# Kernel tuning notes

Hardware: AMD Instinct MI355X
Metric: run time of the kernel (lower is better)

## Reference

```python
import jax, jax.numpy as jnp
import numpy as np

N = 10000      # nodes
E = 320000     # edges (avg degree 32)
C = 256        # feature dim (input_dim == output_dim)
L = 3          # num_layers
D = 20         # KAF dictionary size
BOUNDARY = 4.0 # KAF dictionary boundary


def setup_inputs() -> dict:
    key = jax.random.key(0)
    ks = jax.random.split(key, 7)
    x = jax.random.normal(ks[0], (N, C), jnp.float32)
    edge_index = jax.random.randint(ks[1], (2, E), 0, N, jnp.int32)
    edge_attr = jax.random.normal(ks[2], (E, 2), jnp.float32)
    # per-layer stacked parameters (all layers have identical shapes)
    node_w = jax.random.normal(ks[3], (L, C, C), jnp.float32) / jnp.sqrt(jnp.float32(C))
    edge_w = jax.random.normal(ks[4], (L, 2, C), jnp.float32) / jnp.sqrt(jnp.float32(2))
    neigh_w = jax.random.normal(ks[5], (L, C, C), jnp.float32) / jnp.sqrt(jnp.float32(C))
    bias = jnp.zeros((L, C), jnp.float32)
    alpha = jax.random.normal(ks[6], (L, C, D), jnp.float32) * 0.3
    return dict(x=x, edge_index=edge_index, edge_attr=edge_attr,
                node_w=node_w, edge_w=edge_w, neigh_w=neigh_w, bias=bias, alpha=alpha)


def _kaf(s, alpha_l):
    # Kernel Activation Function (Scardapane et al.): per-channel Gaussian mixture
    dict_pts = jnp.linspace(-BOUNDARY, BOUNDARY, D, dtype=s.dtype)  # [D]
    interval = 2.0 * BOUNDARY / (D - 1)
    gamma = 0.5 / (2.0 * interval) ** 2
    K = jnp.exp(-gamma * jnp.square(s[..., None] - dict_pts))  # [N, C, D]
    return jnp.einsum('ncd,cd->nc', K, alpha_l)


def reference(x, edge_index, edge_attr, node_w, edge_w, neigh_w, bias, alpha):
    src, dst = edge_index[0], edge_index[1]
    # mean-aggregation normalizer (computed once; graph is fixed across layers)
    cnt = jax.ops.segment_sum(jnp.ones((E,), x.dtype), dst, num_segments=N)
    inv_cnt = jnp.where(cnt > 0, 1.0 / jnp.maximum(cnt, 1.0), 0.0)  # [N]
    h = x
    for l in range(L):
        # message: edge_attr @ W_e + x_j @ W_n  -> [E, C]
        msg = edge_attr @ edge_w[l] + h[src] @ neigh_w[l]
        # mean aggregate to destination nodes
        aggr = jax.ops.segment_sum(msg, dst, num_segments=N) * inv_cnt[:, None]
        # update: KAF(aggr + x @ W + b)
        h = _kaf(aggr + h @ node_w[l] + bias[l], alpha[l])
    return h
```

## Files before the change

### kernel.cpp

```cpp
#include <hip/hip_runtime.h>
#include <hip/hip_bf16.h>

#define N_NODES 10000
#define N_EDGES 320000
#define CDIM    256
#define B_PRE   80
#define EPB     (N_EDGES / B_PRE)
#define SLK     130
#define SA      84

typedef __attribute__((ext_vector_type(8))) _Float16 half8;
typedef __attribute__((ext_vector_type(4))) _Float16 half4;
typedef __attribute__((ext_vector_type(4))) float floatx4;

#define OFF_RS    0
#define OFF_INVC  40960
#define OFF_S2    81920
#define OFF_COLV  163840
#define OFF_WCAT  806912
#define OFF_HN    1593344
#define OFF_HX    6713344
#define OFF_PERC  OFF_HN
#define OFF_BASE  (OFF_HN + 1600000)
#define OFF_EA2   OFF_HX
#define OFF_CTOT  (OFF_HX + 2560000)

__global__ __launch_bounds__(256) void k_prep(const float4* __restrict__ x, half4* __restrict__ hB,
                                              const float* __restrict__ neigh_w, const float* __restrict__ node_w,
                                              _Float16* __restrict__ wcatT) {
  __shared__ float t[32][33];
  const int b = blockIdx.x;
  if (b < 2500) {
    int i = b * 256 + threadIdx.x;
    float4 v = x[i];
    half4 h; h.x = (_Float16)v.x; h.y = (_Float16)v.y; h.z = (_Float16)v.z; h.w = (_Float16)v.w;
    hB[i] = h;
    return;
  }
  const int bb = b - 2500;
  const int k0 = (bb & 7) * 32;
  const int n0 = ((bb >> 3) & 15) * 32;
  const int l  = bb >> 7;
  const int tx = threadIdx.x & 31;
  const int ty = threadIdx.x >> 5;
  const float* src = (n0 < 256) ? neigh_w : node_w;
  const int nb = (n0 < 256) ? n0 : (n0 - 256);
#pragma unroll
  for (int p = 0; p < 4; ++p) {
    int k = k0 + ty + p * 8;
    t[ty + p * 8][tx] = src[l * 65536 + k * 256 + (nb + tx)];
  }
  __syncthreads();
#pragma unroll
  for (int p = 0; p < 4; ++p) {
    int n = n0 + ty + p * 8;
    wcatT[(size_t)l * 131072 + n * 256 + (k0 + tx)] = (_Float16)t[tx][ty + p * 8];
  }
}

__global__ __launch_bounds__(1024) void k_count(const int* __restrict__ ei,
                                                unsigned short* __restrict__ percnt) {
  __shared__ int hist[N_NODES];
  const int t = threadIdx.x, b = blockIdx.x;
  for (int n = t; n < N_NODES; n += 1024) hist[n] = 0;
  __syncthreads();
  const int e0 = b * EPB;
  for (int e = e0 + t; e < e0 + EPB; e += 1024)
    atomicAdd(&hist[ei[N_EDGES + e]], 1);
  __syncthreads();
  for (int n = t; n < N_NODES; n += 1024)
    percnt[b * N_NODES + n] = (unsigned short)hist[n];
}

__global__ __launch_bounds__(256) void k_base(const unsigned short* __restrict__ percnt,
                                              int* __restrict__ prefix, int* __restrict__ cnttot) {
  int n = blockIdx.x * 256 + threadIdx.x;
  if (n >= N_NODES) return;
  int s = 0;
  for (int b = 0; b < B_PRE; ++b) {
    prefix[b * N_NODES + n] = s;
    s += (int)percnt[b * N_NODES + n];
  }
  cnttot[n] = s;
}

__global__ __launch_bounds__(1024) void k_scan(const int* __restrict__ cnttot,
                                               int* __restrict__ rs, float* __restrict__ invc) {
  __shared__ int lds[1024];
  const int t = threadIdx.x;
  const int base = t * 10;
  int loc[10];
  int sum = 0;
#pragma unroll
  for (int i = 0; i < 10; ++i) {
    int idx = base + i;
    int v = (idx < N_NODES) ? cnttot[idx] : 0;
    loc[i] = v; sum += v;
  }
  lds[t] = sum; __syncthreads();
  for (int off = 1; off < 1024; off <<= 1) {
    int v = 0;
    if (t >= off) v = lds[t - off];
    __syncthreads();
    if (t >= off) lds[t] += v;
    __syncthreads();
  }
  int ex = lds[t] - sum;
#pragma unroll
  for (int i = 0; i < 10; ++i) {
    int idx = base + i;
    if (idx < N_NODES) {
      rs[idx] = ex; ex += loc[i];
      invc[idx] = (loc[i] > 0) ? (1.0f / (float)loc[i]) : 0.0f;
    }
  }
  if (t == 1023) rs[N_NODES] = lds[1023];
}

__global__ __launch_bounds__(1024) void k_scat(const int* __restrict__ ei, const float* __restrict__ ea,
                                               const int* __restrict__ prefix, const int* __restrict__ rs,
                                               unsigned short* __restrict__ colv, float2* __restrict__ ea2) {
  __shared__ int cur[N_NODES];
  const int t = threadIdx.x, b = blockIdx.x;
  for (int n = t; n < N_NODES; n += 1024)
    cur[n] = rs[n] + prefix[b * N_NODES + n];
  __syncthreads();
  const int e0 = b * EPB;
  for (int e = e0 + t; e < e0 + EPB; e += 1024) {
    int d = ei[N_EDGES + e];
    int src = ei[e];
    float2 a = ((const float2*)ea)[e];
    int pos = atomicAdd(&cur[d], 1);
    colv[pos] = (unsigned short)src;
    ea2[pos] = a;
  }
}

__global__ __launch_bounds__(256) void k_s2(const int* __restrict__ rs, const float2* __restrict__ ea2,
                                            float* __restrict__ s2) {
  int n = blockIdx.x * 256 + threadIdx.x;
  if (n >= N_NODES) return;
  int beg = rs[n], end = rs[n + 1];
  float sx = 0.f, sy = 0.f;
  for (int p = beg; p < end; ++p) { float2 a = ea2[p]; sx += a.x; sy += a.y; }
  s2[2 * n] = sx; s2[2 * n + 1] = sy;
}

__global__ __launch_bounds__(256) void k_gemm(const _Float16* __restrict__ A,
                                              const _Float16* __restrict__ BT,
                                              _Float16* __restrict__ hn,
                                              _Float16* __restrict__ hx) {
  __shared__ _Float16 As[64 * SLK];
  __shared__ _Float16 Bs[64 * SLK];
  const int tid = threadIdx.x;
  const int wv = tid >> 6;
  const int lane = tid & 63;
  const int m0 = blockIdx.x * 64;
  const int n0 = blockIdx.y * 64;
  const int wy = wv >> 1, wx = wv & 1;

  floatx4 acc[2][2];
#pragma unroll
  for (int i = 0; i < 2; ++i)
#pragma unroll
    for (int j = 0; j < 2; ++j) acc[i][j] = (floatx4){0.f, 0.f, 0.f, 0.f};

  const int mrow = 32 * wy + (lane & 15);
  const int nrow = 32 * wx + (lane & 15);
  const int q8 = (lane >> 4) * 8;

#pragma unroll
  for (int kt = 0; kt < 2; ++kt) {
    half8 av[4], bv[4];
#pragma unroll
    for (int c = 0; c < 4; ++c) {
      int ch = tid + 256 * c;
      int row = ch >> 4;
      int off = (ch & 15) * 8;
      int arow = m0 + row; if (arow >= N_NODES) arow = N_NODES - 1;
      av[c] = *(const half8*)(A + (size_t)arow * 256 + kt * 128 + off);
      bv[c] = *(const half8*)(BT + (size_t)(n0 + row) * 256 + kt * 128 + off);
    }
    __syncthreads();
#pragma unroll
    for (int c = 0; c < 4; ++c) {
      int ch = tid + 256 * c;
      int row = ch >> 4;
      int off = (ch & 15) * 8;
      *(half8*)&As[row * SLK + off] = av[c];
      *(half8*)&Bs[row * SLK + off] = bv[c];
    }
    __syncthreads();
#pragma unroll
    for (int ks = 0; ks < 4; ++ks) {
      const int kb = ks * 32 + q8;
      half8 af0 = *(const half8*)&As[mrow * SLK + kb];
      half8 af1 = *(const half8*)&As[(mrow + 16) * SLK + kb];
      half8 bf0 = *(const half8*)&Bs[nrow * SLK + kb];
      half8 bf1 = *(const half8*)&Bs[(nrow + 16) * SLK + kb];
      acc[0][0] = __builtin_amdgcn_mfma_f32_16x16x32_f16(af0, bf0, acc[0][0], 0, 0, 0);
      acc[0][1] = __builtin_amdgcn_mfma_f32_16x16x32_f16(af0, bf1, acc[0][1], 0, 0, 0);
      acc[1][0] = __builtin_amdgcn_mfma_f32_16x16x32_f16(af1, bf0, acc[1][0], 0, 0, 0);
      acc[1][1] = __builtin_amdgcn_mfma_f32_16x16x32_f16(af1, bf1, acc[1][1], 0, 0, 0);
    }
  }

  const int colb = n0 + 32 * wx + (lane & 15);
  const int rowb = m0 + 32 * wy + 4 * (lane >> 4);
#pragma unroll
  for (int i = 0; i < 2; ++i) {
#pragma unroll
    for (int j = 0; j < 2; ++j) {
      const int cn = colb + 16 * j;
#pragma unroll
      for (int r = 0; r < 4; ++r) {
        const int rw = rowb + 16 * i + r;
        if (rw < N_NODES) {
          float v = acc[i][j][r];
          if (cn < 256) hn[rw * 256 + cn] = (_Float16)v;
          else          hx[rw * 256 + (cn - 256)] = (_Float16)v;
        }
      }
    }
  }
}

__global__ __launch_bounds__(256) void k_update(const int* __restrict__ rs, const unsigned short* __restrict__ colv,
                                                const float* __restrict__ invc, const float* __restrict__ s2,
                                                const _Float16* __restrict__ hn, const _Float16* __restrict__ hx,
                                                const float* __restrict__ ew,
                                                const float* __restrict__ bias,
                                                const float* __restrict__ alpha,
                                                _Float16* __restrict__ hmid, float* __restrict__ fout,
                                                int final_layer) {
  __shared__ float alds[64 * SA];
#pragma unroll
  for (int i = 0; i < 20; ++i) {
    int s = threadIdx.x + 256 * i;
    int c = s / 20, j = s - 20 * c;
    alds[(c >> 2) * SA + 4 * j + (c & 3)] = alpha[s];
  }
  __syncthreads();

  const int wv   = threadIdx.x >> 6;
  const int lane = threadIdx.x & 63;
  const int hf   = lane >> 5;
  const int l5   = lane & 31;
  const int n = blockIdx.x * 4 + wv;
  int beg = rs[n], end = rs[n + 1];
  beg = max(0, min(beg, N_EDGES));
  end = max(beg, min(end, N_EDGES));
  const int co = l5 * 8;

  half8 acc0 = (half8)(_Float16)0.f, acc1 = (half8)(_Float16)0.f;
  half8 acc2 = (half8)(_Float16)0.f, acc3 = (half8)(_Float16)0.f;
  for (int base = beg; base < end; base += 64) {
    const int cnt = min(64, end - base);
    int myIdx = 0;
    if (base + lane < end) myIdx = (int)colv[base + lane];
    int j = 0;
    for (; j + 8 <= cnt; j += 8) {
      int s0 = __shfl(myIdx, j + hf);
      int s1 = __shfl(myIdx, j + 2 + hf);
      int s2i = __shfl(myIdx, j + 4 + hf);
      int s3 = __shfl(myIdx, j + 6 + hf);
      half8 v0 = *(const half8*)(hn + (size_t)s0 * 256 + co);
      half8 v1 = *(const half8*)(hn + (size_t)s1 * 256 + co);
      half8 v2 = *(const half8*)(hn + (size_t)s2i * 256 + co);
      half8 v3 = *(const half8*)(hn + (size_t)s3 * 256 + co);
      acc0 += v0; acc1 += v1; acc2 += v2; acc3 += v3;
    }
    for (; j + 2 <= cnt; j += 2) {
      int s0 = __shfl(myIdx, j + hf);
      acc0 += *(const half8*)(hn + (size_t)s0 * 256 + co);
    }
    if (j < cnt) {
      int s0 = __shfl(myIdx, j);
      if (hf == 0)
        acc0 += *(const half8*)(hn + (size_t)s0 * 256 + co);
    }
  }
  acc0 = (acc0 + acc2) + (acc1 + acc3);
  union { half8 h; unsigned int u[4]; } me, ot;
  me.h = acc0;
#pragma unroll
  for (int r = 0; r < 4; ++r) ot.u[r] = (unsigned int)__shfl_xor((int)me.u[r], 32);
  acc0 = me.h + ot.h;

  const int c0 = l5 * 8 + hf * 4;
  float a0, a1, a2, a3;
  if (hf) { a0 = (float)acc0[4]; a1 = (float)acc0[5]; a2 = (float)acc0[6]; a3 = (float)acc0[7]; }
  else    { a0 = (float)acc0[0]; a1 = (float)acc0[1]; a2 = (float)acc0[2]; a3 = (float)acc0[3]; }

  const int q = c0 >> 2;
  const float ic = invc[n];
  const float t0 = s2[2 * n], t1 = s2[2 * n + 1];
  const half4  hv = ((const half4*)hx)[n * 64 + q];
  const float4 e0 = ((const float4*)ew)[q];
  const float4 e1 = ((const float4*)ew)[64 + q];
  const float4 bi = ((const float4*)bias)[q];
  float s[4];
  s[0] = (a0 + t0 * e0.x + t1 * e1.x) * ic + (float)hv.x + bi.x;
  s[1] = (a1 + t0 * e0.y + t1 * e1.y) * ic + (float)hv.y + bi.y;
  s[2] = (a2 + t0 * e0.z + t1 * e1.z) * ic + (float)hv.z + bi.z;
  s[3] = (a3 + t0 * e0.w + t1 * e1.w) * ic + (float)hv.w + bi.w;

  const float G  = -0.705078125f;
  const float WM = 0.7788007831f;
  float K[4], R[4];
#pragma unroll
  for (int k = 0; k < 4; ++k) {
    float t = fminf(fmaxf(s[k], -40.f), 40.f);
    float d = t + 4.0f;
    K[k] = __expf(G * d * d);
    R[k] = __expf(0.59375f * d - 0.125f);
  }
  const float* ar = &alds[q * SA];
  float o0 = 0.f, o1 = 0.f, o2 = 0.f, o3 = 0.f;
#pragma unroll
  for (int j = 0; j < 20; ++j) {
    float4 a4 = *(const float4*)(ar + 4 * j);
    o0 += a4.x * K[0]; o1 += a4.y * K[1]; o2 += a4.z * K[2]; o3 += a4.w * K[3];
    K[0] *= R[0]; K[1] *= R[1]; K[2] *= R[2]; K[3] *= R[3];
    R[0] *= WM;   R[1] *= WM;   R[2] *= WM;   R[3] *= WM;
  }
  if (final_layer) {
    float4 w; w.x = o0; w.y = o1; w.z = o2; w.w = o3;
    ((float4*)fout)[n * 64 + q] = w;
  } else {
    half4 w; w.x = (_Float16)o0; w.y = (_Float16)o1; w.z = (_Float16)o2; w.w = (_Float16)o3;
    ((half4*)hmid)[n * 64 + q] = w;
  }
}

extern "C" void kernel_launch(void* const* d_in, const int* in_sizes, int n_in,
                              void* d_out, int out_size, void* d_ws, size_t ws_size,
                              hipStream_t stream) {
  const float* x       = (const float*)d_in[0];
  const int*   ei      = (const int*)d_in[1];
  const float* ea      = (const float*)d_in[2];
  const float* node_w  = (const float*)d_in[3];
  const float* edge_w  = (const float*)d_in[4];
  const float* neigh_w = (const float*)d_in[5];
  const float* bias    = (const float*)d_in[6];
  const float* alpha   = (const float*)d_in[7];

  char* w = (char*)d_ws;
  int*            rs     = (int*)(w + OFF_RS);
  float*          invc   = (float*)(w + OFF_INVC);
  float*          s2     = (float*)(w + OFF_S2);
  unsigned short* colv   = (unsigned short*)(w + OFF_COLV);
  _Float16*       wcatT  = (_Float16*)(w + OFF_WCAT);
  _Float16*       hn     = (_Float16*)(w + OFF_HN);
  _Float16*       hx     = (_Float16*)(w + OFF_HX);
  unsigned short* percnt = (unsigned short*)(w + OFF_PERC);
  int*            prefix = (int*)(w + OFF_BASE);
  float2*         ea2    = (float2*)(w + OFF_EA2);
  int*            cnttot = (int*)(w + OFF_CTOT);
  float*          fout   = (float*)d_out;
  _Float16*       hB     = (_Float16*)d_out;

  k_prep<<<2884, 256, 0, stream>>>((const float4*)x, (half4*)hB, neigh_w, node_w, wcatT);
  k_count<<<B_PRE, 1024, 0, stream>>>(ei, percnt);
  k_base<<<40, 256, 0, stream>>>(percnt, prefix, cnttot);
  k_scan<<<1, 1024, 0, stream>>>(cnttot, rs, invc);
  k_scat<<<B_PRE, 1024, 0, stream>>>(ei, ea, prefix, rs, colv, ea2);
  k_s2<<<40, 256, 0, stream>>>(rs, ea2, s2);

  for (int l = 0; l < 3; ++l) {
    k_gemm<<<dim3(157, 8, 1), 256, 0, stream>>>(hB, wcatT + l * 131072, hn, hx);
    k_update<<<2500, 256, 0, stream>>>(rs, colv, invc, s2, hn, hx,
                                       edge_w + l * 512, bias + l * 256, alpha + l * 5120,
                                       hB, fout, (l == 2) ? 1 : 0);
  }
}
```

Baseline: 214.6 us.

## Aggregate raw features before GEMM and fuse KAF into concatenated-K GEMM epilogue

Reorders each layer so neighbor features are mean-aggregated first, then a single GEMM over the concatenated [aggregated | self] inputs (K=512) produces all 256 outputs, with the edge-attribute term, bias and KAF activation computed in the GEMM epilogue. This removes the separate update kernel and the fp16 round trip of the intermediate hn/hx buffers. Edge-attribute sums are now accumulated with global float atomics during scatter instead of a separate pass. The trade-off is a larger-K GEMM per tile, per-element scalar stores in the epilogue, and nondeterministic atomic summation order for s2.

```diff
diff --git a/kernel.cpp b/kernel.cpp
--- a/kernel.cpp
+++ b/kernel.cpp
@@ -3,11 +3,9 @@
 
 #define N_NODES 10000
 #define N_EDGES 320000
-#define CDIM    256
 #define B_PRE   80
 #define EPB     (N_EDGES / B_PRE)
 #define SLK     130
-#define SA      84
 
 typedef __attribute__((ext_vector_type(8))) _Float16 half8;
 typedef __attribute__((ext_vector_type(4))) _Float16 half4;
@@ -18,43 +16,48 @@
 #define OFF_S2    81920
 #define OFF_COLV  163840
 #define OFF_WCAT  806912
-#define OFF_HN    1593344
-#define OFF_HX    6713344
-#define OFF_PERC  OFF_HN
-#define OFF_BASE  (OFF_HN + 1600000)
-#define OFF_EA2   OFF_HX
-#define OFF_CTOT  (OFF_HX + 2560000)
-
-__global__ __launch_bounds__(256) void k_prep(const float4* __restrict__ x, half4* __restrict__ hB,
+#define OFF_HA    1593344
+#define OFF_HB    6713344
+#define OFF_G     11833344
+#define OFF_PERC  OFF_G
+#define OFF_BASE  (OFF_G + 1600000)
+#define OFF_CTOT  (OFF_G + 4800000)
+
+__global__ __launch_bounds__(256) void k_prep(const float4* __restrict__ x, half4* __restrict__ hA,
                                               const float* __restrict__ neigh_w, const float* __restrict__ node_w,
-                                              _Float16* __restrict__ wcatT) {
+                                              _Float16* __restrict__ wcatT, float* __restrict__ s2) {
   __shared__ float t[32][33];
   const int b = blockIdx.x;
   if (b < 2500) {
     int i = b * 256 + threadIdx.x;
     float4 v = x[i];
     half4 h; h.x = (_Float16)v.x; h.y = (_Float16)v.y; h.z = (_Float16)v.z; h.w = (_Float16)v.w;
-    hB[i] = h;
+    hA[i] = h;
     return;
   }
+  if (b >= 2884) {
+    int i = (b - 2884) * 256 + threadIdx.x;
+    if (i < 20000) s2[i] = 0.f;
+    return;
+  }
   const int bb = b - 2500;
-  const int k0 = (bb & 7) * 32;
-  const int n0 = ((bb >> 3) & 15) * 32;
+  const int k0 = (bb & 15) * 32;
+  const int n0 = ((bb >> 4) & 7) * 32;
   const int l  = bb >> 7;
   const int tx = threadIdx.x & 31;
   const int ty = threadIdx.x >> 5;
-  const float* src = (n0 < 256) ? neigh_w : node_w;
-  const int nb = (n0 < 256) ? n0 : (n0 - 256);
+  const float* src = (k0 < 256) ? neigh_w : node_w;
+  const int kb = (k0 < 256) ? k0 : (k0 - 256);
 #pragma unroll
   for (int p = 0; p < 4; ++p) {
-    int k = k0 + ty + p * 8;
-    t[ty + p * 8][tx] = src[l * 65536 + k * 256 + (nb + tx)];
+    int k = kb + ty + p * 8;
+    t[ty + p * 8][tx] = src[l * 65536 + k * 256 + (n0 + tx)];
   }
   __syncthreads();
 #pragma unroll
   for (int p = 0; p < 4; ++p) {
     int n = n0 + ty + p * 8;
-    wcatT[(size_t)l * 131072 + n * 256 + (k0 + tx)] = (_Float16)t[tx][ty + p * 8];
+    wcatT[(size_t)l * 131072 + n * 512 + (k0 + tx)] = (_Float16)t[tx][ty + p * 8];
   }
 }
 
@@ -119,7 +122,7 @@
 
 __global__ __launch_bounds__(1024) void k_scat(const int* __restrict__ ei, const float* __restrict__ ea,
                                                const int* __restrict__ prefix, const int* __restrict__ rs,
-                                               unsigned short* __restrict__ colv, float2* __restrict__ ea2) {
+                                               unsigned short* __restrict__ colv, float* __restrict__ s2) {
   __shared__ int cur[N_NODES];
   const int t = threadIdx.x, b = blockIdx.x;
   for (int n = t; n < N_NODES; n += 1024)
@@ -132,116 +135,14 @@
     float2 a = ((const float2*)ea)[e];
     int pos = atomicAdd(&cur[d], 1);
     colv[pos] = (unsigned short)src;
-    ea2[pos] = a;
-  }
-}
-
-__global__ __launch_bounds__(256) void k_s2(const int* __restrict__ rs, const float2* __restrict__ ea2,
-                                            float* __restrict__ s2) {
-  int n = blockIdx.x * 256 + threadIdx.x;
-  if (n >= N_NODES) return;
-  int beg = rs[n], end = rs[n + 1];
-  float sx = 0.f, sy = 0.f;
-  for (int p = beg; p < end; ++p) { float2 a = ea2[p]; sx += a.x; sy += a.y; }
-  s2[2 * n] = sx; s2[2 * n + 1] = sy;
-}
-
-__global__ __launch_bounds__(256) void k_gemm(const _Float16* __restrict__ A,
-                                              const _Float16* __restrict__ BT,
-                                              _Float16* __restrict__ hn,
-                                              _Float16* __restrict__ hx) {
-  __shared__ _Float16 As[64 * SLK];
-  __shared__ _Float16 Bs[64 * SLK];
-  const int tid = threadIdx.x;
-  const int wv = tid >> 6;
-  const int lane = tid & 63;
-  const int m0 = blockIdx.x * 64;
-  const int n0 = blockIdx.y * 64;
-  const int wy = wv >> 1, wx = wv & 1;
-
-  floatx4 acc[2][2];
-#pragma unroll
-  for (int i = 0; i < 2; ++i)
-#pragma unroll
-    for (int j = 0; j < 2; ++j) acc[i][j] = (floatx4){0.f, 0.f, 0.f, 0.f};
-
-  const int mrow = 32 * wy + (lane & 15);
-  const int nrow = 32 * wx + (lane & 15);
-  const int q8 = (lane >> 4) * 8;
-
-#pragma unroll
-  for (int kt = 0; kt < 2; ++kt) {
-    half8 av[4], bv[4];
-#pragma unroll
-    for (int c = 0; c < 4; ++c) {
-      int ch = tid + 256 * c;
-      int row = ch >> 4;
-      int off = (ch & 15) * 8;
-      int arow = m0 + row; if (arow >= N_NODES) arow = N_NODES - 1;
-      av[c] = *(const half8*)(A + (size_t)arow * 256 + kt * 128 + off);
-      bv[c] = *(const half8*)(BT + (size_t)(n0 + row) * 256 + kt * 128 + off);
-    }
-    __syncthreads();
-#pragma unroll
-    for (int c = 0; c < 4; ++c) {
-      int ch = tid + 256 * c;
-      int row = ch >> 4;
-      int off = (ch & 15) * 8;
-      *(half8*)&As[row * SLK + off] = av[c];
-      *(half8*)&Bs[row * SLK + off] = bv[c];
-    }
-    __syncthreads();
-#pragma unroll
-    for (int ks = 0; ks < 4; ++ks) {
-      const int kb = ks * 32 + q8;
-      half8 af0 = *(const half8*)&As[mrow * SLK + kb];
-      half8 af1 = *(const half8*)&As[(mrow + 16) * SLK + kb];
-      half8 bf0 = *(const half8*)&Bs[nrow * SLK + kb];
-      half8 bf1 = *(const half8*)&Bs[(nrow + 16) * SLK + kb];
-      acc[0][0] = __builtin_amdgcn_mfma_f32_16x16x32_f16(af0, bf0, acc[0][0], 0, 0, 0);
-      acc[0][1] = __builtin_amdgcn_mfma_f32_16x16x32_f16(af0, bf1, acc[0][1], 0, 0, 0);
-      acc[1][0] = __builtin_amdgcn_mfma_f32_16x16x32_f16(af1, bf0, acc[1][0], 0, 0, 0);
-      acc[1][1] = __builtin_amdgcn_mfma_f32_16x16x32_f16(af1, bf1, acc[1][1], 0, 0, 0);
-    }
-  }
-
-  const int colb = n0 + 32 * wx + (lane & 15);
-  const int rowb = m0 + 32 * wy + 4 * (lane >> 4);
-#pragma unroll
-  for (int i = 0; i < 2; ++i) {
-#pragma unroll
-    for (int j = 0; j < 2; ++j) {
-      const int cn = colb + 16 * j;
-#pragma unroll
-      for (int r = 0; r < 4; ++r) {
-        const int rw = rowb + 16 * i + r;
-        if (rw < N_NODES) {
-          float v = acc[i][j][r];
-          if (cn < 256) hn[rw * 256 + cn] = (_Float16)v;
-          else          hx[rw * 256 + (cn - 256)] = (_Float16)v;
-        }
-      }
-    }
-  }
-}
-
-__global__ __launch_bounds__(256) void k_update(const int* __restrict__ rs, const unsigned short* __restrict__ colv,
-                                                const float* __restrict__ invc, const float* __restrict__ s2,
-                                                const _Float16* __restrict__ hn, const _Float16* __restrict__ hx,
-                                                const float* __restrict__ ew,
-                                                const float* __restrict__ bias,
-                                                const float* __restrict__ alpha,
-                                                _Float16* __restrict__ hmid, float* __restrict__ fout,
-                                                int final_layer) {
-  __shared__ float alds[64 * SA];
-#pragma unroll
-  for (int i = 0; i < 20; ++i) {
-    int s = threadIdx.x + 256 * i;
-    int c = s / 20, j = s - 20 * c;
-    alds[(c >> 2) * SA + 4 * j + (c & 3)] = alpha[s];
-  }
-  __syncthreads();
-
+    atomicAdd(&s2[2 * d], a.x);
+    atomicAdd(&s2[2 * d + 1], a.y);
+  }
+}
+
+__global__ __launch_bounds__(256) void k_aggr(const int* __restrict__ rs, const unsigned short* __restrict__ colv,
+                                              const float* __restrict__ invc,
+                                              const _Float16* __restrict__ H, _Float16* __restrict__ Gm) {
   const int wv   = threadIdx.x >> 6;
   const int lane = threadIdx.x & 63;
   const int hf   = lane >> 5;
@@ -264,20 +165,20 @@
       int s1 = __shfl(myIdx, j + 2 + hf);
       int s2i = __shfl(myIdx, j + 4 + hf);
       int s3 = __shfl(myIdx, j + 6 + hf);
-      half8 v0 = *(const half8*)(hn + (size_t)s0 * 256 + co);
-      half8 v1 = *(const half8*)(hn + (size_t)s1 * 256 + co);
-      half8 v2 = *(const half8*)(hn + (size_t)s2i * 256 + co);
-      half8 v3 = *(const half8*)(hn + (size_t)s3 * 256 + co);
+      half8 v0 = *(const half8*)(H + (size_t)s0 * 256 + co);
+      half8 v1 = *(const half8*)(H + (size_t)s1 * 256 + co);
+      half8 v2 = *(const half8*)(H + (size_t)s2i * 256 + co);
+      half8 v3 = *(const half8*)(H + (size_t)s3 * 256 + co);
       acc0 += v0; acc1 += v1; acc2 += v2; acc3 += v3;
     }
     for (; j + 2 <= cnt; j += 2) {
       int s0 = __shfl(myIdx, j + hf);
-      acc0 += *(const half8*)(hn + (size_t)s0 * 256 + co);
+      acc0 += *(const half8*)(H + (size_t)s0 * 256 + co);
     }
     if (j < cnt) {
       int s0 = __shfl(myIdx, j);
       if (hf == 0)
-        acc0 += *(const half8*)(hn + (size_t)s0 * 256 + co);
+        acc0 += *(const half8*)(H + (size_t)s0 * 256 + co);
     }
   }
   acc0 = (acc0 + acc2) + (acc1 + acc3);
@@ -287,49 +188,140 @@
   for (int r = 0; r < 4; ++r) ot.u[r] = (unsigned int)__shfl_xor((int)me.u[r], 32);
   acc0 = me.h + ot.h;
 
-  const int c0 = l5 * 8 + hf * 4;
-  float a0, a1, a2, a3;
-  if (hf) { a0 = (float)acc0[4]; a1 = (float)acc0[5]; a2 = (float)acc0[6]; a3 = (float)acc0[7]; }
-  else    { a0 = (float)acc0[0]; a1 = (float)acc0[1]; a2 = (float)acc0[2]; a3 = (float)acc0[3]; }
-
-  const int q = c0 >> 2;
-  const float ic = invc[n];
-  const float t0 = s2[2 * n], t1 = s2[2 * n + 1];
-  const half4  hv = ((const half4*)hx)[n * 64 + q];
-  const float4 e0 = ((const float4*)ew)[q];
-  const float4 e1 = ((const float4*)ew)[64 + q];
-  const float4 bi = ((const float4*)bias)[q];
-  float s[4];
-  s[0] = (a0 + t0 * e0.x + t1 * e1.x) * ic + (float)hv.x + bi.x;
-  s[1] = (a1 + t0 * e0.y + t1 * e1.y) * ic + (float)hv.y + bi.y;
-  s[2] = (a2 + t0 * e0.z + t1 * e1.z) * ic + (float)hv.z + bi.z;
-  s[3] = (a3 + t0 * e0.w + t1 * e1.w) * ic + (float)hv.w + bi.w;
-
-  const float G  = -0.705078125f;
+  if (hf == 0) {
+    const float ic = invc[n];
+    half8 o;
+#pragma unroll
+    for (int k = 0; k < 8; ++k) o[k] = (_Float16)((float)acc0[k] * ic);
+    *(half8*)(Gm + (size_t)n * 256 + co) = o;
+  }
+}
+
+__global__ __launch_bounds__(256) void k_gemm2(const _Float16* __restrict__ Gm,
+                                               const _Float16* __restrict__ Hm,
+                                               const _Float16* __restrict__ BT,
+                                               const float* __restrict__ ew,
+                                               const float* __restrict__ bias,
+                                               const float* __restrict__ alpha,
+                                               const float* __restrict__ invc,
+                                               const float* __restrict__ s2,
+                                               _Float16* __restrict__ hout, float* __restrict__ fout,
+                                               int final_layer) {
+  __shared__ _Float16 As[64 * SLK];
+  __shared__ _Float16 Bs[64 * SLK];
+  __shared__ float alds[64 * 20];
+  const int tid = threadIdx.x;
+  const int wv = tid >> 6;
+  const int lane = tid & 63;
+  const int m0 = blockIdx.x * 64;
+  const int n0 = blockIdx.y * 64;
+  const int wy = wv >> 1, wx = wv & 1;
+
+#pragma unroll
+  for (int ii = 0; ii < 5; ++ii)
+    alds[tid + 256 * ii] = alpha[n0 * 20 + tid + 256 * ii];
+
+  floatx4 acc[2][2];
+#pragma unroll
+  for (int i = 0; i < 2; ++i)
+#pragma unroll
+    for (int j = 0; j < 2; ++j) acc[i][j] = (floatx4){0.f, 0.f, 0.f, 0.f};
+
+  const int mrow = 32 * wy + (lane & 15);
+  const int nrow = 32 * wx + (lane & 15);
+  const int q8 = (lane >> 4) * 8;
+
+#pragma unroll
+  for (int kt = 0; kt < 4; ++kt) {
+    const _Float16* Asrc = (kt < 2) ? Gm : Hm;
+    const int ko = (kt & 1) * 128;
+    half8 av[4], bv[4];
+#pragma unroll
+    for (int c = 0; c < 4; ++c) {
+      int ch = tid + 256 * c;
+      int row = ch >> 4;
+      int off = (ch & 15) * 8;
+      int arow = m0 + row; if (arow >= N_NODES) arow = N_NODES - 1;
+      av[c] = *(const half8*)(Asrc + (size_t)arow * 256 + ko + off);
+      bv[c] = *(const half8*)(BT + (size_t)(n0 + row) * 512 + kt * 128 + off);
+    }
+    __syncthreads();
+#pragma unroll
+    for (int c = 0; c < 4; ++c) {
+      int ch = tid + 256 * c;
+      int row = ch >> 4;
+      int off = (ch & 15) * 8;
+      *(half8*)&As[row * SLK + off] = av[c];
+      *(half8*)&Bs[row * SLK + off] = bv[c];
+    }
+    __syncthreads();
+#pragma unroll
+    for (int ks = 0; ks < 4; ++ks) {
+      const int kb = ks * 32 + q8;
+      half8 af0 = *(const half8*)&As[mrow * SLK + kb];
+      half8 af1 = *(const half8*)&As[(mrow + 16) * SLK + kb];
+      half8 bf0 = *(const half8*)&Bs[nrow * SLK + kb];
+      half8 bf1 = *(const half8*)&Bs[(nrow + 16) * SLK + kb];
+      acc[0][0] = __builtin_amdgcn_mfma_f32_16x16x32_f16(af0, bf0, acc[0][0], 0, 0, 0);
+      acc[0][1] = __builtin_amdgcn_mfma_f32_16x16x32_f16(af0, bf1, acc[0][1], 0, 0, 0);
+      acc[1][0] = __builtin_amdgcn_mfma_f32_16x16x32_f16(af1, bf0, acc[1][0], 0, 0, 0);
+      acc[1][1] = __builtin_amdgcn_mfma_f32_16x16x32_f16(af1, bf1, acc[1][1], 0, 0, 0);
+    }
+  }
+
+  const int rowb = m0 + 32 * wy + 4 * (lane >> 4);
+  const int clb  = 32 * wx + (lane & 15);
+  float icr[2][4], t0r[2][4], t1r[2][4];
+#pragma unroll
+  for (int i = 0; i < 2; ++i)
+#pragma unroll
+    for (int r = 0; r < 4; ++r) {
+      int rw = rowb + 16 * i + r;
+      int rc = (rw < N_NODES) ? rw : (N_NODES - 1);
+      icr[i][r] = invc[rc];
+      t0r[i][r] = s2[2 * rc];
+      t1r[i][r] = s2[2 * rc + 1];
+    }
   const float WM = 0.7788007831f;
-  float K[4], R[4];
-#pragma unroll
-  for (int k = 0; k < 4; ++k) {
-    float t = fminf(fmaxf(s[k], -40.f), 40.f);
-    float d = t + 4.0f;
-    K[k] = __expf(G * d * d);
-    R[k] = __expf(0.59375f * d - 0.125f);
-  }
-  const float* ar = &alds[q * SA];
-  float o0 = 0.f, o1 = 0.f, o2 = 0.f, o3 = 0.f;
-#pragma unroll
-  for (int j = 0; j < 20; ++j) {
-    float4 a4 = *(const float4*)(ar + 4 * j);
-    o0 += a4.x * K[0]; o1 += a4.y * K[1]; o2 += a4.z * K[2]; o3 += a4.w * K[3];
-    K[0] *= R[0]; K[1] *= R[1]; K[2] *= R[2]; K[3] *= R[3];
-    R[0] *= WM;   R[1] *= WM;   R[2] *= WM;   R[3] *= WM;
-  }
-  if (final_layer) {
-    float4 w; w.x = o0; w.y = o1; w.z = o2; w.w = o3;
-    ((float4*)fout)[n * 64 + q] = w;
-  } else {
-    half4 w; w.x = (_Float16)o0; w.y = (_Float16)o1; w.z = (_Float16)o2; w.w = (_Float16)o3;
-    ((half4*)hmid)[n * 64 + q] = w;
+#pragma unroll
+  for (int j = 0; j < 2; ++j) {
+    const int cl = clb + 16 * j;
+    const int cn = n0 + cl;
+    const float e0 = ew[cn], e1 = ew[256 + cn], bi = bias[cn];
+    float a20[20];
+#pragma unroll
+    for (int q = 0; q < 5; ++q)
+      *(float4*)&a20[4 * q] = *(const float4*)&alds[cl * 20 + 4 * q];
+#pragma unroll
+    for (int i = 0; i < 2; ++i) {
+      float K[4], R[4], o[4];
+#pragma unroll
+      for (int r = 0; r < 4; ++r) {
+        float sv = acc[i][j][r] + icr[i][r] * (t0r[i][r] * e0 + t1r[i][r] * e1) + bi;
+        float tt = fminf(fmaxf(sv, -40.f), 40.f);
+        float dd = tt + 4.0f;
+        K[r] = __expf(-0.705078125f * dd * dd);
+        R[r] = __expf(0.59375f * dd - 0.125f);
+        o[r] = 0.f;
+      }
+#pragma unroll
+      for (int d = 0; d < 20; ++d) {
+        o[0] += a20[d] * K[0]; K[0] *= R[0]; R[0] *= WM;
+        o[1] += a20[d] * K[1]; K[1] *= R[1]; R[1] *= WM;
+        o[2] += a20[d] * K[2]; K[2] *= R[2]; R[2] *= WM;
+        o[3] += a20[d] * K[3]; K[3] *= R[3]; R[3] *= WM;
+      }
+      const int rw0 = rowb + 16 * i;
+      if (final_layer) {
+#pragma unroll
+        for (int r = 0; r < 4; ++r)
+          if (rw0 + r < N_NODES) fout[(size_t)(rw0 + r) * 256 + cn] = o[r];
+      } else {
+#pragma unroll
+        for (int r = 0; r < 4; ++r)
+          if (rw0 + r < N_NODES) hout[(size_t)(rw0 + r) * 256 + cn] = (_Float16)o[r];
+      }
+    }
   }
 }
 
@@ -351,26 +343,27 @@
   float*          s2     = (float*)(w + OFF_S2);
   unsigned short* colv   = (unsigned short*)(w + OFF_COLV);
   _Float16*       wcatT  = (_Float16*)(w + OFF_WCAT);
-  _Float16*       hn     = (_Float16*)(w + OFF_HN);
-  _Float16*       hx     = (_Float16*)(w + OFF_HX);
+  _Float16*       hA     = (_Float16*)(w + OFF_HA);
+  _Float16*       hB     = (_Float16*)(w + OFF_HB);
+  _Float16*       g      = (_Float16*)(w + OFF_G);
   unsigned short* percnt = (unsigned short*)(w + OFF_PERC);
   int*            prefix = (int*)(w + OFF_BASE);
-  float2*         ea2    = (float2*)(w + OFF_EA2);
   int*            cnttot = (int*)(w + OFF_CTOT);
   float*          fout   = (float*)d_out;
-  _Float16*       hB     = (_Float16*)d_out;
-
-  k_prep<<<2884, 256, 0, stream>>>((const float4*)x, (half4*)hB, neigh_w, node_w, wcatT);
+
+  k_prep<<<2964, 256, 0, stream>>>((const float4*)x, (half4*)hA, neigh_w, node_w, wcatT, s2);
   k_count<<<B_PRE, 1024, 0, stream>>>(ei, percnt);
   k_base<<<40, 256, 0, stream>>>(percnt, prefix, cnttot);
   k_scan<<<1, 1024, 0, stream>>>(cnttot, rs, invc);
-  k_scat<<<B_PRE, 1024, 0, stream>>>(ei, ea, prefix, rs, colv, ea2);
-  k_s2<<<40, 256, 0, stream>>>(rs, ea2, s2);
-
+  k_scat<<<B_PRE, 1024, 0, stream>>>(ei, ea, prefix, rs, colv, s2);
+
+  _Float16* hin = hA;
   for (int l = 0; l < 3; ++l) {
-    k_gemm<<<dim3(157, 8, 1), 256, 0, stream>>>(hB, wcatT + l * 131072, hn, hx);
-    k_update<<<2500, 256, 0, stream>>>(rs, colv, invc, s2, hn, hx,
-                                       edge_w + l * 512, bias + l * 256, alpha + l * 5120,
-                                       hB, fout, (l == 2) ? 1 : 0);
-  }
-}
+    k_aggr<<<2500, 256, 0, stream>>>(rs, colv, invc, hin, g);
+    _Float16* hout = (l == 0) ? hB : hA;
+    k_gemm2<<<dim3(157, 4), 256, 0, stream>>>(g, hin, wcatT + (size_t)l * 131072,
+                                              edge_w + l * 512, bias + l * 256, alpha + l * 5120,
+                                              invc, s2, hout, fout, (l == 2) ? 1 : 0);
+    hin = hout;
+  }
+}
```

Result: slower. 232.7 us (+8.4%).
